# Optimization experiments

Measured on AMD Instinct MI355X. Metric: run time of the kernel, lower is better.

## Reference

```python
import jax, jax.numpy as jnp
import numpy as np

EMB = 1024
HEADS = 16
DK = EMB // HEADS
EPS = 1e-5


def setup_inputs() -> dict:
    key = jax.random.key(0)
    ks = jax.random.split(key, 7)
    s_in = 1.0 / np.sqrt(EMB)
    return {
        "x": jax.random.normal(ks[0], (4, 2048, EMB), dtype=jnp.float32),
        "W_qkv": jax.random.uniform(ks[1], (EMB, 3 * EMB), jnp.float32, -s_in, s_in),
        "b_qkv": jax.random.uniform(ks[2], (3 * EMB,), jnp.float32, -s_in, s_in),
        "W_out": jax.random.uniform(ks[3], (EMB, EMB), jnp.float32, -s_in, s_in),
        "b_out": jax.random.uniform(ks[4], (EMB,), jnp.float32, -s_in, s_in),
        "gamma": jnp.ones((EMB,), jnp.float32),
        "beta": jnp.zeros((EMB,), jnp.float32),
    }


def reference(x, W_qkv, b_qkv, W_out, b_out, gamma, beta):
    B, T, D = x.shape
    qkv = x @ W_qkv + b_qkv                      # [B,T,3D]
    q, k, v = jnp.split(qkv, 3, axis=-1)
    # [B,T,D] -> [B,H,T,dk]
    def heads(t):
        return t.reshape(B, T, HEADS, DK).transpose(0, 2, 1, 3)
    q, k, v = heads(q), heads(k), heads(v)
    scores = jnp.einsum("bhtd,bhsd->bhts", q, k) / np.sqrt(DK)
    attn = jax.nn.softmax(scores, axis=-1)
    out = jnp.einsum("bhts,bhsd->bhtd", attn, v)  # [B,H,T,dk]
    out = out.transpose(0, 2, 1, 3).reshape(B, T, D)
    out = out @ W_out + b_out
    res = x + out
    mu = jnp.mean(res, axis=-1, keepdims=True)
    var = jnp.mean((res - mu) ** 2, axis=-1, keepdims=True)
    return (res - mu) / jnp.sqrt(var + EPS) * gamma + beta
```

## Files before the change

kernel.cpp:

```cpp
#include <hip/hip_runtime.h>

#define B_ 4
#define T_ 2048
#define D_ 1024
#define H_ 16
#define DK_ 64
#define M_ (B_*T_)

typedef __bf16 bf16;
typedef __bf16 bf16x8 __attribute__((ext_vector_type(8)));
typedef __bf16 bf16x4 __attribute__((ext_vector_type(4)));
typedef short s16x4 __attribute__((ext_vector_type(4)));
typedef float f32x4 __attribute__((ext_vector_type(4)));

__device__ __forceinline__ f32x4 zero4() { f32x4 v = {0.f, 0.f, 0.f, 0.f}; return v; }

__device__ __forceinline__ float fexp2(float x) {
  float r;
  asm("v_exp_f32 %0, %1\n\ts_nop 0" : "=v"(r) : "v"(x));
  return r;
}

__device__ __forceinline__ float max3f(float a, float b, float c) {
  float r;
  asm("v_max3_f32 %0, %1, %2, %3" : "=v"(r) : "v"(a), "v"(b), "v"(c));
  return r;
}

__device__ __forceinline__ void g2l16(const void* g, void* l) {
  __builtin_amdgcn_global_load_lds(
      (const __attribute__((address_space(1))) void*)g,
      (__attribute__((address_space(3))) void*)l, 16, 0, 0);
}

__global__ __launch_bounds__(256) void cast_bf16(const float* __restrict__ src,
                                                 bf16* __restrict__ dst) {
  const size_t i = ((size_t)blockIdx.x * 256 + threadIdx.x) * 8;
  float4 a = *(const float4*)(src + i);
  float4 b = *(const float4*)(src + i + 4);
  bf16x8 v;
  v[0] = (bf16)a.x; v[1] = (bf16)a.y; v[2] = (bf16)a.z; v[3] = (bf16)a.w;
  v[4] = (bf16)b.x; v[5] = (bf16)b.y; v[6] = (bf16)b.z; v[7] = (bf16)b.w;
  *(bf16x8*)(dst + i) = v;
}

__global__ __launch_bounds__(256) void transpose_wf(const float* __restrict__ src,
                                                    bf16* __restrict__ dst, int R, int C) {
  __shared__ alignas(16) bf16 ts[64 * 65];
  const int tid = threadIdx.x;
  const int r0 = blockIdx.x * 64, c0 = blockIdx.y * 64;
  {
    int rr = tid >> 2, cc = (tid & 3) * 16;
    const float4* p4 = (const float4*)(src + (size_t)(r0 + rr) * C + c0 + cc);
    float fv[16];
#pragma unroll
    for (int q = 0; q < 4; ++q) *(float4*)&fv[q * 4] = p4[q];
#pragma unroll
    for (int i = 0; i < 16; ++i) ts[(cc + i) * 65 + rr] = (bf16)fv[i];
  }
  __syncthreads();
  {
    int rr = tid >> 2, cc = (tid & 3) * 16;
    bf16x8 a, b;
#pragma unroll
    for (int i = 0; i < 8; ++i) a[i] = ts[rr * 65 + cc + i];
#pragma unroll
    for (int i = 0; i < 8; ++i) b[i] = ts[rr * 65 + cc + 8 + i];
    bf16* q = dst + (size_t)(c0 + rr) * R + r0 + cc;
    *(bf16x8*)q = a;
    *(bf16x8*)(q + 8) = b;
  }
}

__global__ __launch_bounds__(256) void transpose_v(const bf16* __restrict__ qkv,
                                                   bf16* __restrict__ Vt) {
  __shared__ alignas(16) bf16 ts[64 * 65];
  int bid = blockIdx.x;
  const int tt = bid & 31; bid >>= 5;
  const int h = bid & 15;  const int b = bid >> 4;
  const int t0 = tt * 64;
  const int tid = threadIdx.x;
  {
    int tok = tid >> 2, fc = (tid & 3) * 16;
    const bf16* p = qkv + (size_t)(b * T_ + t0 + tok) * (3 * D_) + 2 * D_ + h * DK_ + fc;
    bf16x8 a = *(const bf16x8*)p;
    bf16x8 c = *(const bf16x8*)(p + 8);
#pragma unroll
    for (int i = 0; i < 8; ++i) ts[(fc + i) * 65 + tok] = a[i];
#pragma unroll
    for (int i = 0; i < 8; ++i) ts[(fc + 8 + i) * 65 + tok] = c[i];
  }
  __syncthreads();
  {
    int f = tid >> 2, tc = (tid & 3) * 16;
    bf16x8 a, c;
#pragma unroll
    for (int i = 0; i < 8; ++i) a[i] = ts[f * 65 + tc + i];
#pragma unroll
    for (int i = 0; i < 8; ++i) c[i] = ts[f * 65 + tc + 8 + i];
    bf16* q = Vt + ((size_t)(b * H_ + h) * DK_ + f) * T_ + t0 + tc;
    *(bf16x8*)q = a;
    *(bf16x8*)(q + 8) = c;
  }
}

template <bool FUSE>
__global__ __launch_bounds__(256) void gemm64(const bf16* __restrict__ A,
                                              const bf16* __restrict__ Bt,
                                              const float* __restrict__ bias,
                                              bf16* __restrict__ Cbf,
                                              float* __restrict__ Cf,
                                              const float* __restrict__ resid,
                                              int N, int K, int lda, int ldc) {
  __shared__ alignas(16) bf16 As[128 * 64];
  __shared__ alignas(16) bf16 Bs[128 * 64];
  const int tid = threadIdx.x;
  const int wid = tid >> 6, lane = tid & 63, quad = lane >> 4, l16 = lane & 15;
  const int m0 = blockIdx.x * 128, n0 = blockIdx.y * 128;
  const int wr = (wid >> 1) * 64, wc = (wid & 1) * 64;
  const int sw = l16 & 7;

  f32x4 acc[4][4];
#pragma unroll
  for (int i = 0; i < 4; ++i)
#pragma unroll
    for (int j = 0; j < 4; ++j) acc[i][j] = zero4();

  for (int k0 = 0; k0 < K; k0 += 64) {
    __syncthreads();
#pragma unroll
    for (int p = 0; p < 4; ++p) {
      const int t = p * 256 + tid;
      const int row = t >> 3;
      const int kcs = ((t & 7) ^ (row & 7)) * 8;
      g2l16(Bt + (size_t)(n0 + row) * K + k0 + kcs, (char*)Bs + p * 4096 + wid * 1024);
      g2l16(A + (size_t)(m0 + row) * lda + k0 + kcs, (char*)As + p * 4096 + wid * 1024);
    }
    __syncthreads();
#pragma unroll
    for (int kk = 0; kk < 2; ++kk) {
      bf16x8 af[4], bfr[4];
#pragma unroll
      for (int i = 0; i < 4; ++i)
        af[i] = *(const bf16x8*)&As[(wr + i * 16 + l16) * 64 + ((((kk << 2) | quad) ^ sw) * 8)];
#pragma unroll
      for (int j = 0; j < 4; ++j)
        bfr[j] = *(const bf16x8*)&Bs[(wc + j * 16 + l16) * 64 + ((((kk << 2) | quad) ^ sw) * 8)];
#pragma unroll
      for (int i = 0; i < 4; ++i)
#pragma unroll
        for (int j = 0; j < 4; ++j)
          acc[i][j] = __builtin_amdgcn_mfma_f32_16x16x32_bf16(af[i], bfr[j], acc[i][j], 0, 0, 0);
    }
  }

#pragma unroll
  for (int i = 0; i < 4; ++i) {
#pragma unroll
    for (int j = 0; j < 4; ++j) {
      const int col = n0 + wc + j * 16 + l16;
      const float bv = bias[col];
#pragma unroll
      for (int r = 0; r < 4; ++r) {
        const int row = m0 + wr + i * 16 + quad * 4 + r;
        const float v = acc[i][j][r] + bv;
        if (FUSE) {
          const size_t off = (size_t)row * N + col;
          Cf[off] = v + resid[off];
        } else {
          Cbf[(size_t)row * ldc + col] = (bf16)v;
        }
      }
    }
  }
}

__global__ __launch_bounds__(256, 4) void attn_db(const bf16* __restrict__ qkv,
                                                  const bf16* __restrict__ Vt,
                                                  bf16* __restrict__ out) {
  __shared__ alignas(16) bf16 Ks[2][64 * 64];
  __shared__ alignas(16) bf16 Vs[2][64 * 64];
  const int tid = threadIdx.x;
  const int wid = tid >> 6, lane = tid & 63, quad = lane >> 4, l16 = lane & 15;
  const int bid = blockIdx.x;
  const int qb = bid & 15, h = (bid >> 4) & 15, b = bid >> 8;
  const int q0 = qb * 128;

  const int lrow8 = lane >> 3;
  const int kch = (lane & 7) ^ lrow8;
  const bf16* kg = qkv + (size_t)(b * T_ + wid * 16 + lrow8) * (3 * D_) + D_ + h * DK_ + kch * 8;
  const bf16* vg = Vt + ((size_t)(b * H_ + h) * DK_ + wid * 16 + lrow8) * T_ + kch * 8;

  const float SC = 0.125f * 1.44269504f;
  bf16x8 qA[2], qB[2];
  {
    const bf16* qpA = qkv + (size_t)(b * T_ + q0 + wid * 32 + l16) * (3 * D_) + h * DK_ + quad * 8;
    const bf16* qpB = qpA + (size_t)16 * (3 * D_);
    qA[0] = *(const bf16x8*)qpA;       qA[1] = *(const bf16x8*)(qpA + 32);
    qB[0] = *(const bf16x8*)qpB;       qB[1] = *(const bf16x8*)(qpB + 32);
#pragma unroll
    for (int i = 0; i < 8; ++i) {
      qA[0][i] = (bf16)((float)qA[0][i] * SC); qA[1][i] = (bf16)((float)qA[1][i] * SC);
      qB[0][i] = (bf16)((float)qB[0][i] * SC); qB[1][i] = (bf16)((float)qB[1][i] * SC);
    }
  }

  float miA = -1e30f, miB = -1e30f;
  f32x4 liA4 = zero4(), liB4 = zero4();
  f32x4 oA[4], oB[4];
#pragma unroll
  for (int ft = 0; ft < 4; ++ft) { oA[ft] = zero4(); oB[ft] = zero4(); }

  auto stage = [&](int buf, int t0) {
    g2l16(kg + (size_t)(t0 + 0) * (3 * D_), &Ks[buf][(wid * 16 + 0) * 64]);
    g2l16(kg + (size_t)(t0 + 8) * (3 * D_), &Ks[buf][(wid * 16 + 8) * 64]);
    g2l16(vg + (size_t)0 * T_ + t0,         &Vs[buf][(wid * 16 + 0) * 64]);
    g2l16(vg + (size_t)8 * T_ + t0,         &Vs[buf][(wid * 16 + 8) * 64]);
  };

  stage(0, 0);
  __syncthreads();

  for (int kt = 0; kt < T_ / 64; ++kt) {
    const int cur = kt & 1;
    if (kt + 1 < T_ / 64) stage(cur ^ 1, (kt + 1) * 64);

    f32x4 svA[4], svB[4];
#pragma unroll
    for (int nt = 0; nt < 4; ++nt) { svA[nt] = zero4(); svB[nt] = zero4(); }
    __builtin_amdgcn_s_setprio(1);
#pragma unroll
    for (int nt = 0; nt < 4; ++nt)
#pragma unroll
      for (int ks = 0; ks < 2; ++ks) {
        const bf16x8 kf = *(const bf16x8*)
            &Ks[cur][(nt * 16 + l16) * 64 + (((ks << 2) | quad) ^ (l16 & 7)) * 8];
        svA[nt] = __builtin_amdgcn_mfma_f32_16x16x32_bf16(kf, qA[ks], svA[nt], 0, 0, 0);
        svB[nt] = __builtin_amdgcn_mfma_f32_16x16x32_bf16(kf, qB[ks], svB[nt], 0, 0, 0);
      }
    __builtin_amdgcn_s_setprio(0);

    float a0 = max3f(svA[0][0], svA[0][1], svA[0][2]);
    float a1 = max3f(svA[0][3], svA[1][0], svA[1][1]);
    a0 = max3f(a0, svA[1][2], svA[1][3]);
    a1 = max3f(a1, svA[2][0], svA[2][1]);
    a0 = max3f(a0, svA[2][2], svA[2][3]);
    a1 = max3f(a1, svA[3][0], svA[3][1]);
    a0 = max3f(a0, svA[3][2], svA[3][3]);
    float b0 = max3f(svB[0][0], svB[0][1], svB[0][2]);
    float b1 = max3f(svB[0][3], svB[1][0], svB[1][1]);
    b0 = max3f(b0, svB[1][2], svB[1][3]);
    b1 = max3f(b1, svB[2][0], svB[2][1]);
    b0 = max3f(b0, svB[2][2], svB[2][3]);
    b1 = max3f(b1, svB[3][0], svB[3][1]);
    b0 = max3f(b0, svB[3][2], svB[3][3]);
    const float tAl = fmaxf(a0, a1), tBl = fmaxf(b0, b1);

    if (!__all(tAl <= miA + 8.f)) {
      float tA = fmaxf(tAl, __shfl_xor(tAl, 16, 64));
      tA = fmaxf(tA, __shfl_xor(tA, 32, 64));
      const float nm = fmaxf(miA, tA);
      const float al = fexp2(miA - nm);
      miA = nm; liA4 *= al;
#pragma unroll
      for (int r = 0; r < 4; ++r) {
        const float ar = __shfl(al, quad * 4 + r, 64);
#pragma unroll
        for (int ft = 0; ft < 4; ++ft) oA[ft][r] *= ar;
      }
    }
    if (!__all(tBl <= miB + 8.f)) {
      float tB = fmaxf(tBl, __shfl_xor(tBl, 16, 64));
      tB = fmaxf(tB, __shfl_xor(tB, 32, 64));
      const float nm = fmaxf(miB, tB);
      const float al = fexp2(miB - nm);
      miB = nm; liB4 *= al;
#pragma unroll
      for (int r = 0; r < 4; ++r) {
        const float ar = __shfl(al, quad * 4 + r, 64);
#pragma unroll
        for (int ft = 0; ft < 4; ++ft) oB[ft][r] *= ar;
      }
    }

    s16x4 pA[4], pB[4];
#pragma unroll
    for (int nt = 0; nt < 4; ++nt) {
      f32x4 dA = svA[nt] - miA;
      dA[0] = fexp2(dA[0]); dA[1] = fexp2(dA[1]); dA[2] = fexp2(dA[2]); dA[3] = fexp2(dA[3]);
      liA4 += dA;
      union { bf16x4 b; s16x4 s; } ua;
#pragma unroll
      for (int j = 0; j < 4; ++j) ua.b[j] = (bf16)dA[j];
      pA[nt] = ua.s;
      f32x4 dB = svB[nt] - miB;
      dB[0] = fexp2(dB[0]); dB[1] = fexp2(dB[1]); dB[2] = fexp2(dB[2]); dB[3] = fexp2(dB[3]);
      liB4 += dB;
      union { bf16x4 b; s16x4 s; } ub;
#pragma unroll
      for (int j = 0; j < 4; ++j) ub.b[j] = (bf16)dB[j];
      pB[nt] = ub.s;
    }

    __builtin_amdgcn_s_setprio(1);
#pragma unroll
    for (int ks = 0; ks < 4; ++ks)
#pragma unroll
      for (int ft = 0; ft < 4; ++ft) {
        const s16x4 vf = *(const s16x4*)
            &Vs[cur][(ft * 16 + l16) * 64 +
                     ((ks * 2 + (quad >> 1)) ^ (l16 & 7)) * 8 + (quad & 1) * 4];
        oA[ft] = __builtin_amdgcn_mfma_f32_16x16x16bf16_1k(pA[ks], vf, oA[ft], 0, 0, 0);
        oB[ft] = __builtin_amdgcn_mfma_f32_16x16x16bf16_1k(pB[ks], vf, oB[ft], 0, 0, 0);
      }
    __builtin_amdgcn_s_setprio(0);

    __syncthreads();
  }

  float sA = (liA4[0] + liA4[1]) + (liA4[2] + liA4[3]);
  sA += __shfl_xor(sA, 16, 64);
  sA += __shfl_xor(sA, 32, 64);
  float sB = (liB4[0] + liB4[1]) + (liB4[2] + liB4[3]);
  sB += __shfl_xor(sB, 16, 64);
  sB += __shfl_xor(sB, 32, 64);

#pragma unroll
  for (int r = 0; r < 4; ++r) {
    const float invA = 1.0f / __shfl(sA, quad * 4 + r, 64);
    const float invB = 1.0f / __shfl(sB, quad * 4 + r, 64);
    const int rowA = b * T_ + q0 + wid * 32 + quad * 4 + r;
    const int rowB = rowA + 16;
#pragma unroll
    for (int ft = 0; ft < 4; ++ft) {
      out[(size_t)rowA * (3 * D_) + h * DK_ + ft * 16 + l16] = (bf16)(oA[ft][r] * invA);
      out[(size_t)rowB * (3 * D_) + h * DK_ + ft * 16 + l16] = (bf16)(oB[ft][r] * invB);
    }
  }
}

__global__ __launch_bounds__(256) void ln_out(float* __restrict__ res,
                                              const float* __restrict__ gamma,
                                              const float* __restrict__ beta) {
  const int row = blockIdx.x * 4 + (threadIdx.x >> 6);
  const int lane = threadIdx.x & 63;
  float4 v[4];
  float s = 0.f, q = 0.f;
#pragma unroll
  for (int p = 0; p < 4; ++p) {
    v[p] = *(const float4*)(res + (size_t)row * D_ + p * 256 + lane * 4);
    s += v[p].x + v[p].y + v[p].z + v[p].w;
    q += v[p].x * v[p].x + v[p].y * v[p].y + v[p].z * v[p].z + v[p].w * v[p].w;
  }
#pragma unroll
  for (int m = 1; m < 64; m <<= 1) { s += __shfl_xor(s, m, 64); q += __shfl_xor(q, m, 64); }
  const float mu = s * (1.0f / D_);
  const float var = q * (1.0f / D_) - mu * mu;
  const float rstd = rsqrtf(var + 1e-5f);
#pragma unroll
  for (int p = 0; p < 4; ++p) {
    const int c = p * 256 + lane * 4;
    const float4 g = *(const float4*)(gamma + c);
    const float4 be = *(const float4*)(beta + c);
    float4 ov;
    ov.x = (v[p].x - mu) * rstd * g.x + be.x;
    ov.y = (v[p].y - mu) * rstd * g.y + be.y;
    ov.z = (v[p].z - mu) * rstd * g.z + be.z;
    ov.w = (v[p].w - mu) * rstd * g.w + be.w;
    *(float4*)(res + (size_t)row * D_ + c) = ov;
  }
}

extern "C" void kernel_launch(void* const* d_in, const int* in_sizes, int n_in,
                              void* d_out, int out_size, void* d_ws, size_t ws_size,
                              hipStream_t stream) {
  const float* x     = (const float*)d_in[0];
  const float* Wqkv  = (const float*)d_in[1];
  const float* bqkv  = (const float*)d_in[2];
  const float* Wout  = (const float*)d_in[3];
  const float* bout  = (const float*)d_in[4];
  const float* gamma = (const float*)d_in[5];
  const float* beta  = (const float*)d_in[6];
  float* out = (float*)d_out;

  char* ws = (char*)d_ws;
  bf16* WqkvT = (bf16*)ws; ws += (size_t)3 * D_ * D_ * 2;
  bf16* WoutT = (bf16*)ws; ws += (size_t)D_ * D_ * 2;
  bf16* qkv   = (bf16*)ws; ws += (size_t)M_ * 3 * D_ * 2;
  bf16* Vt    = (bf16*)ws;
  bf16* attn  = qkv + 2 * D_;
  bf16* xb    = Vt;

  transpose_wf<<<dim3(D_ / 64, 3 * D_ / 64), 256, 0, stream>>>(Wqkv, WqkvT, D_, 3 * D_);
  transpose_wf<<<dim3(D_ / 64, D_ / 64), 256, 0, stream>>>(Wout, WoutT, D_, D_);
  cast_bf16<<<M_ * D_ / (256 * 8), 256, 0, stream>>>(x, xb);
  gemm64<false><<<dim3(M_ / 128, 3 * D_ / 128), 256, 0, stream>>>(
      xb, WqkvT, bqkv, qkv, nullptr, nullptr, 3 * D_, D_, D_, 3 * D_);
  transpose_v<<<B_ * H_ * (T_ / 64), 256, 0, stream>>>(qkv, Vt);
  attn_db<<<B_ * H_ * (T_ / 128), 256, 0, stream>>>(qkv, Vt, attn);
  gemm64<true><<<dim3(M_ / 128, D_ / 128), 256, 0, stream>>>(
      attn, WoutT, bout, nullptr, out, x, D_, D_, 3 * D_, D_);
  ln_out<<<M_ / 4, 256, 0, stream>>>(out, gamma, beta);
}
```

Baseline: 307.5 us.

## Drop V transpose kernel; read V via transposing LDS loads in attention

Removes the separate transpose_v kernel and stages V tiles directly from the qkv buffer into LDS in row layout, then uses ds_read_b64_tr_b16 to obtain the transposed fragments for the PV MFMAs. Attention output is written to a dense [M,D] buffer instead of into the qkv slots, and block indices are remapped so that neighbouring blocks are spread across heads and batches. This saves one kernel launch and a full read/write pass over V, at the cost of an explicit lgkmcnt wait before the MFMAs and reliance on the transpose-read instruction.

```diff
diff --git a/kernel.cpp b/kernel.cpp
--- a/kernel.cpp
+++ b/kernel.cpp
@@ -69,38 +69,6 @@
     bf16* q = dst + (size_t)(c0 + rr) * R + r0 + cc;
     *(bf16x8*)q = a;
     *(bf16x8*)(q + 8) = b;
-  }
-}
-
-__global__ __launch_bounds__(256) void transpose_v(const bf16* __restrict__ qkv,
-                                                   bf16* __restrict__ Vt) {
-  __shared__ alignas(16) bf16 ts[64 * 65];
-  int bid = blockIdx.x;
-  const int tt = bid & 31; bid >>= 5;
-  const int h = bid & 15;  const int b = bid >> 4;
-  const int t0 = tt * 64;
-  const int tid = threadIdx.x;
-  {
-    int tok = tid >> 2, fc = (tid & 3) * 16;
-    const bf16* p = qkv + (size_t)(b * T_ + t0 + tok) * (3 * D_) + 2 * D_ + h * DK_ + fc;
-    bf16x8 a = *(const bf16x8*)p;
-    bf16x8 c = *(const bf16x8*)(p + 8);
-#pragma unroll
-    for (int i = 0; i < 8; ++i) ts[(fc + i) * 65 + tok] = a[i];
-#pragma unroll
-    for (int i = 0; i < 8; ++i) ts[(fc + 8 + i) * 65 + tok] = c[i];
-  }
-  __syncthreads();
-  {
-    int f = tid >> 2, tc = (tid & 3) * 16;
-    bf16x8 a, c;
-#pragma unroll
-    for (int i = 0; i < 8; ++i) a[i] = ts[f * 65 + tc + i];
-#pragma unroll
-    for (int i = 0; i < 8; ++i) c[i] = ts[f * 65 + tc + 8 + i];
-    bf16* q = Vt + ((size_t)(b * H_ + h) * DK_ + f) * T_ + t0 + tc;
-    *(bf16x8*)q = a;
-    *(bf16x8*)(q + 8) = c;
   }
 }
 
@@ -176,20 +144,23 @@
 }
 
 __global__ __launch_bounds__(256, 4) void attn_db(const bf16* __restrict__ qkv,
-                                                  const bf16* __restrict__ Vt,
-                                                  bf16* __restrict__ out) {
-  __shared__ alignas(16) bf16 Ks[2][64 * 64];
-  __shared__ alignas(16) bf16 Vs[2][64 * 64];
+                                                  bf16* __restrict__ ao) {
+  __shared__ alignas(16) bf16 Ks[2][4096];
+  __shared__ alignas(16) bf16 Vs2[2][4096];
   const int tid = threadIdx.x;
   const int wid = tid >> 6, lane = tid & 63, quad = lane >> 4, l16 = lane & 15;
-  const int bid = blockIdx.x;
+  const int bid0 = blockIdx.x;
+  const int bid = ((bid0 & 7) << 7) | (bid0 >> 3);
   const int qb = bid & 15, h = (bid >> 4) & 15, b = bid >> 8;
   const int q0 = qb * 128;
 
   const int lrow8 = lane >> 3;
   const int kch = (lane & 7) ^ lrow8;
   const bf16* kg = qkv + (size_t)(b * T_ + wid * 16 + lrow8) * (3 * D_) + D_ + h * DK_ + kch * 8;
-  const bf16* vg = Vt + ((size_t)(b * H_ + h) * DK_ + wid * 16 + lrow8) * T_ + kch * 8;
+  const int vtok = (lane >> 5) * 4 + ((lane >> 1) & 3);
+  const int vfof = ((lane >> 3) & 3) * 16 + (lane & 1) * 8;
+  const bf16* vg = qkv + (size_t)(b * T_ + vtok) * (3 * D_) + 2 * D_ + h * DK_ + vfof;
+  const unsigned vbase = (unsigned)(uintptr_t)&Vs2[0][0];
 
   const float SC = 0.125f * 1.44269504f;
   bf16x8 qA[2], qB[2];
@@ -214,8 +185,8 @@
   auto stage = [&](int buf, int t0) {
     g2l16(kg + (size_t)(t0 + 0) * (3 * D_), &Ks[buf][(wid * 16 + 0) * 64]);
     g2l16(kg + (size_t)(t0 + 8) * (3 * D_), &Ks[buf][(wid * 16 + 8) * 64]);
-    g2l16(vg + (size_t)0 * T_ + t0,         &Vs[buf][(wid * 16 + 0) * 64]);
-    g2l16(vg + (size_t)8 * T_ + t0,         &Vs[buf][(wid * 16 + 8) * 64]);
+    g2l16(vg + (size_t)(t0 + 0) * (3 * D_),  (char*)&Vs2[buf][0] + (0 + wid * 2) * 512);
+    g2l16(vg + (size_t)(t0 + 32) * (3 * D_), (char*)&Vs2[buf][0] + (8 + wid * 2) * 512);
   };
 
   stage(0, 0);
@@ -303,16 +274,24 @@
     }
 
     __builtin_amdgcn_s_setprio(1);
-#pragma unroll
-    for (int ks = 0; ks < 4; ++ks)
-#pragma unroll
-      for (int ft = 0; ft < 4; ++ft) {
-        const s16x4 vf = *(const s16x4*)
-            &Vs[cur][(ft * 16 + l16) * 64 +
-                     ((ks * 2 + (quad >> 1)) ^ (l16 & 7)) * 8 + (quad & 1) * 4];
-        oA[ft] = __builtin_amdgcn_mfma_f32_16x16x16bf16_1k(pA[ks], vf, oA[ft], 0, 0, 0);
-        oB[ft] = __builtin_amdgcn_mfma_f32_16x16x16bf16_1k(pB[ks], vf, oB[ft], 0, 0, 0);
-      }
+    {
+      const unsigned va = vbase + (unsigned)cur * 8192u + (unsigned)(quad * 512 + l16 * 8);
+#pragma unroll
+      for (int ks = 0; ks < 4; ++ks) {
+        s16x4 vf[4];
+#pragma unroll
+        for (int ft = 0; ft < 4; ++ft)
+          asm volatile("ds_read_b64_tr_b16 %0, %1 offset:%2"
+                       : "=v"(vf[ft]) : "v"(va), "i"(ks * 2048 + ft * 128));
+        asm volatile("s_waitcnt lgkmcnt(0)" ::: "memory");
+        __builtin_amdgcn_sched_barrier(0);
+#pragma unroll
+        for (int ft = 0; ft < 4; ++ft) {
+          oA[ft] = __builtin_amdgcn_mfma_f32_16x16x16bf16_1k(pA[ks], vf[ft], oA[ft], 0, 0, 0);
+          oB[ft] = __builtin_amdgcn_mfma_f32_16x16x16bf16_1k(pB[ks], vf[ft], oB[ft], 0, 0, 0);
+        }
+      }
+    }
     __builtin_amdgcn_s_setprio(0);
 
     __syncthreads();
@@ -333,8 +312,8 @@
     const int rowB = rowA + 16;
 #pragma unroll
     for (int ft = 0; ft < 4; ++ft) {
-      out[(size_t)rowA * (3 * D_) + h * DK_ + ft * 16 + l16] = (bf16)(oA[ft][r] * invA);
-      out[(size_t)rowB * (3 * D_) + h * DK_ + ft * 16 + l16] = (bf16)(oB[ft][r] * invB);
+      ao[(size_t)rowA * D_ + h * DK_ + ft * 16 + l16] = (bf16)(oA[ft][r] * invA);
+      ao[(size_t)rowB * D_ + h * DK_ + ft * 16 + l16] = (bf16)(oB[ft][r] * invB);
     }
   }
 }
@@ -387,18 +366,16 @@
   bf16* WqkvT = (bf16*)ws; ws += (size_t)3 * D_ * D_ * 2;
   bf16* WoutT = (bf16*)ws; ws += (size_t)D_ * D_ * 2;
   bf16* qkv   = (bf16*)ws; ws += (size_t)M_ * 3 * D_ * 2;
-  bf16* Vt    = (bf16*)ws;
-  bf16* attn  = qkv + 2 * D_;
-  bf16* xb    = Vt;
+  bf16* ao    = (bf16*)ws;
+  bf16* xb    = ao;
 
   transpose_wf<<<dim3(D_ / 64, 3 * D_ / 64), 256, 0, stream>>>(Wqkv, WqkvT, D_, 3 * D_);
   transpose_wf<<<dim3(D_ / 64, D_ / 64), 256, 0, stream>>>(Wout, WoutT, D_, D_);
   cast_bf16<<<M_ * D_ / (256 * 8), 256, 0, stream>>>(x, xb);
   gemm64<false><<<dim3(M_ / 128, 3 * D_ / 128), 256, 0, stream>>>(
       xb, WqkvT, bqkv, qkv, nullptr, nullptr, 3 * D_, D_, D_, 3 * D_);
-  transpose_v<<<B_ * H_ * (T_ / 64), 256, 0, stream>>>(qkv, Vt);
-  attn_db<<<B_ * H_ * (T_ / 128), 256, 0, stream>>>(qkv, Vt, attn);
+  attn_db<<<B_ * H_ * (T_ / 128), 256, 0, stream>>>(qkv, ao);
   gemm64<true><<<dim3(M_ / 128, D_ / 128), 256, 0, stream>>>(
-      attn, WoutT, bout, nullptr, out, x, D_, D_, 3 * D_, D_);
+      ao, WoutT, bout, nullptr, out, x, D_, D_, D_, D_);
   ln_out<<<M_ / 4, 256, 0, stream>>>(out, gamma, beta);
 }
```

After: 299.9 us. -2.5%, faster.
